# Optimization experiments

Hardware: AMD Instinct MI355X
Metric: run time of the kernel (lower is better)

Reference implementation:

```python
import jax, jax.numpy as jnp
import numpy as np
from jax import lax

T = 32768
DUNITS = 1024
ATT_DIM = 512
EPROJS = 512
ACONV_CHANS = 32
ACONV_FILTS = 15  # kernel = 2*15+1 = 31


def setup_inputs() -> dict:
    key = jax.random.key(0)
    ks = jax.random.split(key, 8)
    dec_z = jax.random.normal(ks[0], (1, DUNITS), jnp.float32)
    att_prev = jax.random.uniform(ks[1], (1, T), jnp.float32)
    att_prev = att_prev / jnp.sum(att_prev, axis=1, keepdims=True)  # prob-like alignment
    pre_compute_enc_h = jax.random.normal(ks[2], (1, T, ATT_DIM), jnp.float32) * 0.1
    enc_h = jax.random.normal(ks[3], (1, T, EPROJS), jnp.float32)
    mask = jnp.zeros((1, T), jnp.float32)  # additive mask (0 = keep)
    conv_w = jax.random.normal(ks[4], (ACONV_CHANS, 1, 2 * ACONV_FILTS + 1), jnp.float32) * 0.1
    conv_b = jnp.zeros((ACONV_CHANS,), jnp.float32)
    W_att = jax.random.normal(ks[5], (ATT_DIM, ACONV_CHANS), jnp.float32) * 0.1
    W_dec = jax.random.normal(ks[6], (ATT_DIM, DUNITS), jnp.float32) * 0.03
    W_g = jax.random.normal(ks[7], (1, ATT_DIM), jnp.float32) * 0.05
    b_g = jnp.zeros((1,), jnp.float32)
    return {"dec_z": dec_z, "att_prev": att_prev, "pre_compute_enc_h": pre_compute_enc_h,
            "enc_h": enc_h, "mask": mask, "conv_w": conv_w, "conv_b": conv_b,
            "W_att": W_att, "W_dec": W_dec, "W_g": W_g, "b_g": b_g}


def reference(dec_z, att_prev, pre_compute_enc_h, enc_h, mask, conv_w, conv_b, W_att, W_dec, W_g, b_g):
    scaling = 2.0
    # location conv: att_prev [1,T] -> [1,C,T] (Conv2d with height-1 kernel == Conv1d)
    att_conv = lax.conv_general_dilated(
        att_prev[:, None, :], conv_w, window_strides=(1,),
        padding=[(ACONV_FILTS, ACONV_FILTS)],
        dimension_numbers=("NCH", "OIH", "NCH"))
    att_conv = att_conv + conv_b[None, :, None]          # [1,C,T]
    att_conv = jnp.einsum("bct,ac->bta", att_conv, W_att)  # mlp_att -> [1,T,att_dim]
    dec_z_tiled = (dec_z @ W_dec.T)[:, None, :]           # [1,1,att_dim]
    # gvec over tanh sum -> energies [1,T]
    e = jnp.einsum("bta,a->bt", jnp.tanh(pre_compute_enc_h + dec_z_tiled + att_conv), W_g[0]) + b_g[0]
    e = e + mask
    w = jax.nn.softmax(scaling * e, axis=1)               # [1,T]
    # forward-attention recurrence: shift-add-mul, then L1 normalize
    att_prev_shift = jnp.pad(att_prev, ((0, 0), (1, 0)))[:, :-1]
    w = (att_prev + att_prev_shift) * w
    w = jnp.clip(w, 1e-6, None)
    w = w / jnp.sum(w, axis=1, keepdims=True)             # L1 normalize (w > 0)
    c = jnp.sum(enc_h * w[:, :, None], axis=1)            # [1,eprojs]
    return (c, w)
```

## Files before the change

kernel.cpp:

```cpp
#include <hip/hip_runtime.h>

#define T_LEN 32768
#define ADIM  512
#define NDEC  1024
#define KTAPS 31

#define WS_BASE 0
#define WS_G    512
#define WS_SARR 16384
#define WS_BMAX 49152
#define WS_BSUM 51200
#define WS_SSUM 53248
#define WS_U    53504
#define WS_CREP 86272

typedef __attribute__((ext_vector_type(8))) short bf16x8;
typedef __attribute__((ext_vector_type(4))) float f32x4;

__device__ __forceinline__ float fast_tanh(float x) {
    float e = __expf(2.0f * x);
    return 1.0f - 2.0f * __builtin_amdgcn_rcpf(e + 1.0f);
}

__device__ __forceinline__ unsigned short f2bf(float f) {
    unsigned u = __float_as_uint(f);
    return (unsigned short)((u + 0x7FFFu + ((u >> 16) & 1u)) >> 16);
}

__global__ __launch_bounds__(256) void k0_prep(
        const float* __restrict__ dec_z, const float* __restrict__ conv_w,
        const float* __restrict__ conv_b, const float* __restrict__ W_att,
        const float* __restrict__ W_dec, float* __restrict__ ws) {
    int b = blockIdx.x, tid = threadIdx.x;
    int lane = tid & 63, wave = tid >> 6;
    if (b < 64) {
        if (b == 0 && tid == 0) ws[WS_SSUM] = 0.f;
        for (int s = 0; s < 2; ++s) {
            int a = b * 8 + wave * 2 + s;
            float sum = 0.f;
            #pragma unroll
            for (int i = 0; i < 16; ++i)
                sum += W_dec[a * NDEC + i * 64 + lane] * dec_z[i * 64 + lane];
            #pragma unroll
            for (int off = 32; off > 0; off >>= 1) sum += __shfl_xor(sum, off);
            if (lane == 0) {
                float bias = 0.f;
                #pragma unroll
                for (int c = 0; c < 32; ++c) bias += conv_b[c] * W_att[a * 32 + c];
                ws[WS_BASE + a] = sum + bias;
            }
        }
    } else {
        int k = b - 64;
        unsigned short* Gf = (unsigned short*)(ws + WS_G);
        for (int s = 0; s < 2; ++s) {
            int a = 2 * tid + s;
            float g = 0.f;
            if (k < KTAPS) {
                #pragma unroll
                for (int c = 0; c < 32; ++c)
                    g += conv_w[c * KTAPS + k] * W_att[a * 32 + c];
            }
            int at = a >> 4, col = a & 15;
            int l = col | ((k >> 3) << 4), i = k & 7;
            Gf[(at * 64 + l) * 8 + i] = f2bf(g);
        }
    }
}

__global__ __launch_bounds__(512, 6) void k1_energy(
        const float* __restrict__ att_prev, const float* __restrict__ pre,
        const float* __restrict__ mask, const float* __restrict__ W_g,
        const float* __restrict__ b_g, float* __restrict__ ws) {
    __shared__ float pre_s[16 * ADIM];
    __shared__ float ap_s[48];
    __shared__ float eP[8][16];
    int tid = threadIdx.x, lane = tid & 63, wave = tid >> 6;
    int t0 = blockIdx.x * 16;

    if (blockIdx.x < 32) ws[WS_CREP + blockIdx.x * 512 + tid] = 0.f;

    {
        const float* grow = pre + (size_t)(t0 + 2 * wave) * ADIM + lane * 4;
        float* lrow = &pre_s[(2 * wave) * ADIM];
        #pragma unroll
        for (int r = 0; r < 2; ++r) {
            #pragma unroll
            for (int h = 0; h < 2; ++h) {
                __builtin_amdgcn_global_load_lds(
                    (const __attribute__((address_space(1))) void*)(grow + r * ADIM + h * 256),
                    (__attribute__((address_space(3))) void*)(lrow + r * ADIM + h * 256),
                    16, 0, 0);
            }
        }
    }
    if (tid < 48) {
        int g = t0 - 15 + tid;
        ap_s[tid] = (g >= 0 && g < T_LEN) ? att_prev[g] : 0.f;
    }
    __syncthreads();

    int row = lane & 15, g4 = lane >> 4;

    bf16x8 afrag;
    int aidx = row + g4 * 8;
    #pragma unroll
    for (int i = 0; i < 8; ++i) afrag[i] = (short)f2bf(ap_s[aidx + i]);

    const unsigned short* Gf = (const unsigned short*)(ws + WS_G);
    float e_acc[4] = {0.f, 0.f, 0.f, 0.f};

    #pragma unroll 2
    for (int p = 0; p < 4; ++p) {
        int at = wave * 4 + p;
        int ac = at * 16 + row;
        bf16x8 bfrag = *(const bf16x8*)(Gf + (size_t)(at * 64 + lane) * 8);
        float bs = ws[WS_BASE + ac];
        f32x4 c = {bs, bs, bs, bs};
        c = __builtin_amdgcn_mfma_f32_16x16x32_bf16(afrag, bfrag, c, 0, 0, 0);
        float wgv = W_g[ac];
        #pragma unroll
        for (int r = 0; r < 4; ++r) {
            float pv = pre_s[(g4 * 4 + r) * ADIM + ac];
            e_acc[r] = fmaf(fast_tanh(c[r] + pv), wgv, e_acc[r]);
        }
    }

    #pragma unroll
    for (int r = 0; r < 4; ++r) {
        float s = e_acc[r];
        s += __shfl_xor(s, 1); s += __shfl_xor(s, 2);
        s += __shfl_xor(s, 4); s += __shfl_xor(s, 8);
        e_acc[r] = s;
    }
    if (row == 0) {
        #pragma unroll
        for (int r = 0; r < 4; ++r) eP[wave][g4 * 4 + r] = e_acc[r];
    }
    __syncthreads();

    if (wave == 0) {
        float sv = -1e30f, z0 = 0.f;
        if (lane < 16) {
            float e = 0.f;
            #pragma unroll
            for (int q = 0; q < 8; ++q) e += eP[q][lane];
            int t = t0 + lane;
            sv = 2.0f * (e + b_g[0] + mask[t]);
            ws[WS_SARR + t] = sv;
            z0 = 1.0f;
        }
        float m = sv, z = z0;
        #pragma unroll
        for (int off = 32; off > 0; off >>= 1) {
            float mo = __shfl_xor(m, off), zo = __shfl_xor(z, off);
            float mn = fmaxf(m, mo);
            z = z * __expf(m - mn) + zo * __expf(mo - mn);
            m = mn;
        }
        if (lane == 0) { ws[WS_BMAX + blockIdx.x] = m; ws[WS_BSUM + blockIdx.x] = z; }
    }
}

__global__ __launch_bounds__(512) void k3_context(
        const float* __restrict__ att_prev, const float* __restrict__ enc_h,
        float* __restrict__ ws) {
    __shared__ float wmz[16];
    __shared__ float cbuf[4 * 512];
    int tid = threadIdx.x, lane = tid & 63, wave = tid >> 6;

    float m = -1e30f, z = 0.f;
    int base = wave * 256 + lane;
    #pragma unroll
    for (int q = 0; q < 4; ++q) {
        float mo = ws[WS_BMAX + base + q * 64], zo = ws[WS_BSUM + base + q * 64];
        float mn = fmaxf(m, mo);
        z = z * __expf(m - mn) + zo * __expf(mo - mn);
        m = mn;
    }
    #pragma unroll
    for (int off = 32; off > 0; off >>= 1) {
        float mo = __shfl_xor(m, off), zo = __shfl_xor(z, off);
        float mn = fmaxf(m, mo);
        z = z * __expf(m - mn) + zo * __expf(mo - mn);
        m = mn;
    }
    if (lane == 0) { wmz[wave] = m; wmz[8 + wave] = z; }
    __syncthreads();
    float M = wmz[0], Z = wmz[8];
    #pragma unroll
    for (int w = 1; w < 8; ++w) {
        float mn = fmaxf(M, wmz[w]);
        Z = Z * __expf(M - mn) + wmz[8 + w] * __expf(wmz[w] - mn);
        M = mn;
    }
    float invZ = 1.0f / Z;

    int t0 = blockIdx.x * 32;
    int team = tid >> 7, l = tid & 127;
    int a4 = 4 * l;
    int tbase = t0 + team * 8;
    float4 acc = make_float4(0.f, 0.f, 0.f, 0.f);
    #pragma unroll
    for (int i = 0; i < 8; ++i) {
        int t = tbase + i;
        float ap0 = att_prev[t];
        float apm = (t > 0) ? att_prev[t - 1] : 0.f;
        float u = fmaxf((ap0 + apm) * __expf(ws[WS_SARR + t] - M) * invZ, 1e-6f);
        float4 e = *(const float4*)(enc_h + (size_t)t * ADIM + a4);
        acc.x = fmaf(u, e.x, acc.x);
        acc.y = fmaf(u, e.y, acc.y);
        acc.z = fmaf(u, e.z, acc.z);
        acc.w = fmaf(u, e.w, acc.w);
    }
    if (team != 0) *(float4*)&cbuf[team * 512 + a4] = acc;

    if (tid < 32) {
        int t = t0 + tid;
        float ap0 = att_prev[t];
        float apm = (t > 0) ? att_prev[t - 1] : 0.f;
        float u = fmaxf((ap0 + apm) * __expf(ws[WS_SARR + t] - M) * invZ, 1e-6f);
        ws[WS_U + t] = u;
        float s = u;
        #pragma unroll
        for (int off = 16; off > 0; off >>= 1) s += __shfl_xor(s, off, 32);
        if (tid == 0) atomicAdd(&ws[WS_SSUM], s);
    }
    __syncthreads();
    if (team == 0) {
        float4 b1 = *(const float4*)&cbuf[1 * 512 + a4];
        float4 b2 = *(const float4*)&cbuf[2 * 512 + a4];
        float4 b3 = *(const float4*)&cbuf[3 * 512 + a4];
        float* rep = ws + WS_CREP + (blockIdx.x & 31) * 512;
        atomicAdd(&rep[a4 + 0], acc.x + b1.x + b2.x + b3.x);
        atomicAdd(&rep[a4 + 1], acc.y + b1.y + b2.y + b3.y);
        atomicAdd(&rep[a4 + 2], acc.z + b1.z + b2.z + b3.z);
        atomicAdd(&rep[a4 + 3], acc.w + b1.w + b2.w + b3.w);
    }
}

__global__ __launch_bounds__(512) void k4_final(
        const float* __restrict__ ws, float* __restrict__ out) {
    int b = blockIdx.x, tid = threadIdx.x;
    float invS = 1.0f / ws[WS_SSUM];
    if (b == 0) {
        float acc = 0.f;
        #pragma unroll
        for (int r = 0; r < 32; ++r) acc += ws[WS_CREP + r * 512 + tid];
        out[tid] = acc * invS;
    } else {
        int i = (b - 1) * 512 + tid;
        out[512 + i] = ws[WS_U + i] * invS;
    }
}

extern "C" void kernel_launch(void* const* d_in, const int* in_sizes, int n_in,
                              void* d_out, int out_size, void* d_ws, size_t ws_size,
                              hipStream_t stream) {
    const float* dec_z    = (const float*)d_in[0];
    const float* att_prev = (const float*)d_in[1];
    const float* pre      = (const float*)d_in[2];
    const float* enc_h    = (const float*)d_in[3];
    const float* mask     = (const float*)d_in[4];
    const float* conv_w   = (const float*)d_in[5];
    const float* conv_b   = (const float*)d_in[6];
    const float* W_att    = (const float*)d_in[7];
    const float* W_dec    = (const float*)d_in[8];
    const float* W_g      = (const float*)d_in[9];
    const float* b_g      = (const float*)d_in[10];
    float* out = (float*)d_out;
    float* ws  = (float*)d_ws;

    k0_prep   <<<96,   256, 0, stream>>>(dec_z, conv_w, conv_b, W_att, W_dec, ws);
    k1_energy <<<2048, 512, 0, stream>>>(att_prev, pre, mask, W_g, b_g, ws);
    k3_context<<<1024, 512, 0, stream>>>(att_prev, enc_h, ws);
    k4_final  <<<65,   512, 0, stream>>>(ws, out);
}
```

Baseline: 183.3 us.

## Stage enc_h tiles into LDS via direct loads and simplify context reduction

The context kernel now copies each block's 32 enc_h rows straight into shared memory with global_load_lds. Each wave recomputes the global softmax max and sum on its own, which removes the cross-wave shared-memory merge and one barrier. The attention weights are then broadcast by lane shuffles while each thread accumulates one output column over the 32 timesteps. The energy kernel's launch-bounds occupancy hint is raised from 6 to 8. In exchange, shared memory per block grows to 64KB, which limits how many blocks fit per CU, and the softmax-statistics reduction is repeated in every wave.

After: 183.6 us. About the same (+0.2%).

```diff
diff --git a/kernel.cpp b/kernel.cpp
--- a/kernel.cpp
+++ b/kernel.cpp
@@ -68,7 +68,7 @@
     }
 }
 
-__global__ __launch_bounds__(512, 6) void k1_energy(
+__global__ __launch_bounds__(512, 8) void k1_energy(
         const float* __restrict__ att_prev, const float* __restrict__ pre,
         const float* __restrict__ mask, const float* __restrict__ W_g,
         const float* __restrict__ b_g, float* __restrict__ ws) {
@@ -165,15 +165,30 @@
 __global__ __launch_bounds__(512) void k3_context(
         const float* __restrict__ att_prev, const float* __restrict__ enc_h,
         float* __restrict__ ws) {
-    __shared__ float wmz[16];
-    __shared__ float cbuf[4 * 512];
+    __shared__ float enc_s[32 * ADIM];
     int tid = threadIdx.x, lane = tid & 63, wave = tid >> 6;
+    int t0 = blockIdx.x * 32;
+
+    {
+        const float* grow = enc_h + (size_t)(t0 + 4 * wave) * ADIM + lane * 4;
+        float* lrow = &enc_s[(4 * wave) * ADIM];
+        #pragma unroll
+        for (int r = 0; r < 4; ++r) {
+            #pragma unroll
+            for (int h = 0; h < 2; ++h) {
+                __builtin_amdgcn_global_load_lds(
+                    (const __attribute__((address_space(1))) void*)(grow + r * ADIM + h * 256),
+                    (__attribute__((address_space(3))) void*)(lrow + r * ADIM + h * 256),
+                    16, 0, 0);
+            }
+        }
+    }
 
     float m = -1e30f, z = 0.f;
-    int base = wave * 256 + lane;
-    #pragma unroll
-    for (int q = 0; q < 4; ++q) {
-        float mo = ws[WS_BMAX + base + q * 64], zo = ws[WS_BSUM + base + q * 64];
+    #pragma unroll 8
+    for (int q = 0; q < 32; ++q) {
+        float mo = ws[WS_BMAX + q * 64 + lane];
+        float zo = ws[WS_BSUM + q * 64 + lane];
         float mn = fmaxf(m, mo);
         z = z * __expf(m - mn) + zo * __expf(mo - mn);
         m = mn;
@@ -185,58 +200,31 @@
         z = z * __expf(m - mn) + zo * __expf(mo - mn);
         m = mn;
     }
-    if (lane == 0) { wmz[wave] = m; wmz[8 + wave] = z; }
-    __syncthreads();
-    float M = wmz[0], Z = wmz[8];
-    #pragma unroll
-    for (int w = 1; w < 8; ++w) {
-        float mn = fmaxf(M, wmz[w]);
-        Z = Z * __expf(M - mn) + wmz[8 + w] * __expf(wmz[w] - mn);
-        M = mn;
-    }
-    float invZ = 1.0f / Z;
-
-    int t0 = blockIdx.x * 32;
-    int team = tid >> 7, l = tid & 127;
-    int a4 = 4 * l;
-    int tbase = t0 + team * 8;
-    float4 acc = make_float4(0.f, 0.f, 0.f, 0.f);
-    #pragma unroll
-    for (int i = 0; i < 8; ++i) {
-        int t = tbase + i;
+    float invZ = 1.0f / z;
+
+    float u = 0.f;
+    if (lane < 32) {
+        int t = t0 + lane;
         float ap0 = att_prev[t];
         float apm = (t > 0) ? att_prev[t - 1] : 0.f;
-        float u = fmaxf((ap0 + apm) * __expf(ws[WS_SARR + t] - M) * invZ, 1e-6f);
-        float4 e = *(const float4*)(enc_h + (size_t)t * ADIM + a4);
-        acc.x = fmaf(u, e.x, acc.x);
-        acc.y = fmaf(u, e.y, acc.y);
-        acc.z = fmaf(u, e.z, acc.z);
-        acc.w = fmaf(u, e.w, acc.w);
-    }
-    if (team != 0) *(float4*)&cbuf[team * 512 + a4] = acc;
-
-    if (tid < 32) {
-        int t = t0 + tid;
-        float ap0 = att_prev[t];
-        float apm = (t > 0) ? att_prev[t - 1] : 0.f;
-        float u = fmaxf((ap0 + apm) * __expf(ws[WS_SARR + t] - M) * invZ, 1e-6f);
-        ws[WS_U + t] = u;
-        float s = u;
+        u = fmaxf((ap0 + apm) * __expf(ws[WS_SARR + t] - m) * invZ, 1e-6f);
+    }
+    if (wave == 0) {
+        if (lane < 32) ws[WS_U + t0 + lane] = u;
+        float s = (lane < 32) ? u : 0.f;
         #pragma unroll
         for (int off = 16; off > 0; off >>= 1) s += __shfl_xor(s, off, 32);
-        if (tid == 0) atomicAdd(&ws[WS_SSUM], s);
-    }
+        if (lane == 0) atomicAdd(&ws[WS_SSUM], s);
+    }
+
     __syncthreads();
-    if (team == 0) {
-        float4 b1 = *(const float4*)&cbuf[1 * 512 + a4];
-        float4 b2 = *(const float4*)&cbuf[2 * 512 + a4];
-        float4 b3 = *(const float4*)&cbuf[3 * 512 + a4];
-        float* rep = ws + WS_CREP + (blockIdx.x & 31) * 512;
-        atomicAdd(&rep[a4 + 0], acc.x + b1.x + b2.x + b3.x);
-        atomicAdd(&rep[a4 + 1], acc.y + b1.y + b2.y + b3.y);
-        atomicAdd(&rep[a4 + 2], acc.z + b1.z + b2.z + b3.z);
-        atomicAdd(&rep[a4 + 3], acc.w + b1.w + b2.w + b3.w);
-    }
+
+    int a = wave * 64 + lane;
+    float acc = 0.f;
+    #pragma unroll
+    for (int t = 0; t < 32; ++t)
+        acc = fmaf(__shfl(u, t), enc_s[t * ADIM + a], acc);
+    atomicAdd(&ws[WS_CREP + (blockIdx.x & 31) * 512 + a], acc);
 }
 
 __global__ __launch_bounds__(512) void k4_final(
```
